# Performance work log

Measured on AMD Instinct MI355X. Metric: run time of the kernel, lower is better.

The kernel has to match this reference:

```python
import jax, jax.numpy as jnp
import numpy as np

D_MODEL = 512
NUM_HEADS = 8


def setup_inputs() -> dict:
    key = jax.random.key(0)
    ks = jax.random.split(key, 12)
    B, S, D = 2, 4096, D_MODEL
    scale = 1.0 / np.sqrt(D)
    inp = {
        "q": jax.random.normal(ks[0], (B, S, D), jnp.float32),
        "k": jax.random.normal(ks[1], (B, S, D), jnp.float32),
        "v": jax.random.normal(ks[2], (B, S, D), jnp.float32),
        "w_q": jax.random.normal(ks[3], (D, D), jnp.float32) * scale,
        "b_q": jax.random.normal(ks[4], (D,), jnp.float32) * scale,
        "w_k": jax.random.normal(ks[5], (D, D), jnp.float32) * scale,
        "b_k": jax.random.normal(ks[6], (D,), jnp.float32) * scale,
        "w_v": jax.random.normal(ks[7], (D, D), jnp.float32) * scale,
        "b_v": jax.random.normal(ks[8], (D,), jnp.float32) * scale,
        "w_o": jax.random.normal(ks[9], (D, D), jnp.float32) * scale,
        "b_o": jax.random.normal(ks[10], (D,), jnp.float32) * scale,
    }
    return inp


def _split_heads(x, h):
    b, s, d = x.shape
    return x.reshape(b, s, h, d // h).transpose(0, 2, 1, 3)  # [B,H,S,dk]


def reference(q, k, v, w_q, b_q, w_k, b_k, w_v, b_v, w_o, b_o):
    h = NUM_HEADS
    # Linear projections (torch Linear: x @ W.T + b)
    qh = _split_heads(q @ w_q.T + b_q, h)
    kh = _split_heads(k @ w_k.T + b_k, h)
    vh = _split_heads(v @ w_v.T + b_v, h)
    d_k = kh.shape[-1]
    scores = jnp.einsum("bhsd,bhtd->bhst", qh, kh) / jnp.sqrt(jnp.float32(d_k))
    attn = jax.nn.softmax(scores, axis=-1)  # [B,H,S,S] - materialized, as in source
    out = jnp.einsum("bhst,bhtd->bhsd", attn, vh)
    b, _, s, dk = out.shape
    out = out.transpose(0, 2, 1, 3).reshape(b, s, h * dk)
    return out @ w_o.T + b_o
```

## Files before the change

kernel.cpp:

```cpp
#include <hip/hip_runtime.h>
#include <hip/hip_bf16.h>

#define D_MODEL 512
#define NHEAD   8
#define DK      64
#define SEQ     4096
#define BATCH   2
#define NTOK    (BATCH * SEQ)

typedef __bf16 bf16;
typedef __bf16 bf16x2 __attribute__((ext_vector_type(2)));
typedef __bf16 bf16x4 __attribute__((ext_vector_type(4)));
typedef __bf16 bf16x8 __attribute__((ext_vector_type(8)));
typedef float  f32x4  __attribute__((ext_vector_type(4)));
typedef float  f32x16 __attribute__((ext_vector_type(16)));
typedef unsigned u32x4 __attribute__((ext_vector_type(4)));

#define MFMA16(a, b, c) __builtin_amdgcn_mfma_f32_16x16x32_bf16((a), (b), (c), 0, 0, 0)
#define MFMA32(a, b, c) __builtin_amdgcn_mfma_f32_32x32x16_bf16((a), (b), (c), 0, 0, 0)

#define QSCALE 0.18033688f

__device__ __forceinline__ unsigned pkbf16(float a, float b) {
    bf16x2 t = {(bf16)a, (bf16)b};
    return __builtin_bit_cast(unsigned, t);
}

__global__ __launch_bounds__(256) void cvt_w(
    const float* __restrict__ wq, const float* __restrict__ wk,
    const float* __restrict__ wv, const float* __restrict__ wo,
    bf16* __restrict__ Wb)
{
    int i = blockIdx.x * 256 + threadIdx.x;
    int m = i >> 16;
    int g = i & 65535;
    const float* src = (m == 0) ? wq : (m == 1) ? wk : (m == 2) ? wv : wo;
    float4 x = *(const float4*)(src + (size_t)g * 4);
    bf16x4 y = {(bf16)x.x, (bf16)x.y, (bf16)x.z, (bf16)x.w};
    *(bf16x4*)(Wb + (size_t)m * D_MODEL * D_MODEL + (size_t)g * 4) = y;
}

__global__ __launch_bounds__(256, 3) void proj_qkv(
    const float* __restrict__ q, const float* __restrict__ k, const float* __restrict__ v,
    const bf16* __restrict__ Wb,
    const float* __restrict__ bq, const float* __restrict__ bk, const float* __restrict__ bv,
    bf16* __restrict__ Qh, bf16* __restrict__ Kh, bf16* __restrict__ Vt)
{
    const int p = blockIdx.z;
    const float* X    = (p == 0) ? q  : (p == 1) ? k  : v;
    const bf16*  W    = Wb + (size_t)p * D_MODEL * D_MODEL;
    const float* bias = (p == 0) ? bq : (p == 1) ? bk : bv;

    __shared__ union __align__(16) {
        struct { bf16 As[128][72]; bf16 Bs[128][72]; } g;
        bf16 T[128][136];
    } sm;

    const int m0   = blockIdx.x * 128;
    const int n0   = blockIdx.y * 128;
    const int tid  = threadIdx.x;
    const int lane = tid & 63;
    const int wave = tid >> 6;
    const int low4 = lane & 15;
    const int quad = lane >> 4;
    const int wm   = wave >> 1;
    const int wn   = wave & 1;

    int srow[8], sc4[8];
    for (int it = 0; it < 8; ++it) {
        int idx = tid + it * 256;
        srow[it] = idx >> 4;
        sc4[it]  = (idx & 15) * 4;
    }
    int br[4], bc[4];
    for (int it = 0; it < 4; ++it) {
        int idx = tid + it * 256;
        br[it] = idx >> 3;
        bc[it] = (idx & 7) * 8;
    }

    float4 gA[8];
    bf16x8 gB[4];
    for (int it = 0; it < 8; ++it)
        gA[it] = *(const float4*)(X + (size_t)(m0 + srow[it]) * D_MODEL + sc4[it]);
    for (int it = 0; it < 4; ++it)
        gB[it] = *(const bf16x8*)(W + (size_t)(n0 + br[it]) * D_MODEL + bc[it]);

    f32x4 acc[4][4];
    for (int i = 0; i < 4; ++i)
        for (int j = 0; j < 4; ++j)
            acc[i][j] = f32x4{0.f, 0.f, 0.f, 0.f};

    for (int k0 = 0; k0 < D_MODEL; k0 += 64) {
        __syncthreads();
        for (int it = 0; it < 8; ++it) {
            bf16x4 wa = {(bf16)gA[it].x, (bf16)gA[it].y, (bf16)gA[it].z, (bf16)gA[it].w};
            *(bf16x4*)&sm.g.As[srow[it]][sc4[it]] = wa;
        }
        for (int it = 0; it < 4; ++it)
            *(bf16x8*)&sm.g.Bs[br[it]][bc[it]] = gB[it];
        __syncthreads();

        if (k0 + 64 < D_MODEL) {
            for (int it = 0; it < 8; ++it)
                gA[it] = *(const float4*)(X + (size_t)(m0 + srow[it]) * D_MODEL + k0 + 64 + sc4[it]);
            for (int it = 0; it < 4; ++it)
                gB[it] = *(const bf16x8*)(W + (size_t)(n0 + br[it]) * D_MODEL + k0 + 64 + bc[it]);
        }

        for (int ks = 0; ks < 2; ++ks) {
            bf16x8 a[4], b[4];
            for (int i = 0; i < 4; ++i)
                a[i] = *(const bf16x8*)&sm.g.As[wm * 64 + i * 16 + low4][ks * 32 + quad * 8];
            for (int j = 0; j < 4; ++j)
                b[j] = *(const bf16x8*)&sm.g.Bs[wn * 64 + j * 16 + low4][ks * 32 + quad * 8];
            for (int i = 0; i < 4; ++i)
                for (int j = 0; j < 4; ++j)
                    acc[i][j] = MFMA16(a[i], b[j], acc[i][j]);
        }
    }

    if (p < 2) {
        bf16* Out = (p == 0) ? Qh : Kh;
        const float sc = (p == 0) ? QSCALE : 1.0f;
        for (int j = 0; j < 4; ++j) {
            int col = n0 + wn * 64 + j * 16 + low4;
            float bcol = bias[col];
            for (int i = 0; i < 4; ++i)
                for (int r = 0; r < 4; ++r) {
                    int row = m0 + wm * 64 + i * 16 + quad * 4 + r;
                    Out[(size_t)row * D_MODEL + col] = (bf16)((acc[i][j][r] + bcol) * sc);
                }
        }
    } else {
        __syncthreads();
        for (int j = 0; j < 4; ++j) {
            int col = n0 + wn * 64 + j * 16 + low4;
            float bcol = bias[col];
            for (int i = 0; i < 4; ++i)
                for (int r = 0; r < 4; ++r)
                    sm.T[wn * 64 + j * 16 + low4][wm * 64 + i * 16 + quad * 4 + r] =
                        (bf16)(acc[i][j][r] + bcol);
        }
        __syncthreads();
        const int bb = m0 >> 12;
        const int s0 = (m0 & 4095);
        for (int it = 0; it < 8; ++it) {
            int cc = it * 16 + (tid >> 4);
            int ml = (tid & 15) * 8;
            int col = n0 + cc;
            int hh = col >> 6, dd = col & 63;
            *(bf16x8*)&Vt[(((size_t)(bb * NHEAD + hh) * DK + dd) << 12) + s0 + ml] =
                *(const bf16x8*)&sm.T[cc][ml];
        }
    }
}

__global__ __launch_bounds__(512, 2) void attn(
    const bf16* __restrict__ Qh, const bf16* __restrict__ Kh,
    const bf16* __restrict__ Vt, bf16* __restrict__ O)
{
    __shared__ union __align__(16) {
        struct { bf16 Ks[128][72]; bf16 Vs[64][136]; } s;
        float Obuf[4][32][68];
    } sm;
    __shared__ float Lbuf[4][32];

    const int q0   = blockIdx.x * 128;
    const int bh   = blockIdx.y;
    const int b    = bh >> 3, h = bh & 7;
    const int tid  = threadIdx.x;
    const int lane = tid & 63;
    const int wave = tid >> 6;
    const int qg   = wave >> 1;
    const int kg   = wave & 1;
    const int m32  = lane & 31;
    const int hl   = lane >> 5;

    const bf16* Kbase = Kh + (size_t)b * SEQ * D_MODEL + h * DK;
    const bf16* Vbase = Vt + (size_t)bh * DK * SEQ;

    const bf16* Qrow = Qh + (size_t)(b * SEQ + q0 + qg * 32 + m32) * D_MODEL + h * DK;
    bf16x8 qf[4];
    for (int ks = 0; ks < 4; ++ks)
        qf[ks] = *(const bf16x8*)(Qrow + ks * 16 + hl * 8);

    float l = 0.f;
    f32x16 acc[2];
    for (int i = 0; i < 16; ++i) { acc[0][i] = 0.f; acc[1][i] = 0.f; }

    int kr[2], kc[2], vr[2], vc[2];
    for (int it = 0; it < 2; ++it) {
        int c = tid + it * 512;
        kr[it] = c >> 3;  kc[it] = (c & 7) * 8;
        vr[it] = c >> 4;  vc[it] = (c & 15) * 8;
    }
    bf16x8 gk[2], gv[2];
    for (int it = 0; it < 2; ++it) {
        gk[it] = *(const bf16x8*)(Kbase + (size_t)kr[it] * D_MODEL + kc[it]);
        gv[it] = *(const bf16x8*)(Vbase + (size_t)vr[it] * SEQ + vc[it]);
    }

    for (int t0 = 0; t0 < SEQ; t0 += 128) {
        __syncthreads();
        for (int it = 0; it < 2; ++it) {
            *(bf16x8*)&sm.s.Ks[kr[it]][kc[it]] = gk[it];
            *(bf16x8*)&sm.s.Vs[vr[it]][vc[it]] = gv[it];
        }
        __syncthreads();

        if (t0 + 128 < SEQ) {
            for (int it = 0; it < 2; ++it) {
                gk[it] = *(const bf16x8*)(Kbase + (size_t)(t0 + 128 + kr[it]) * D_MODEL + kc[it]);
                gv[it] = *(const bf16x8*)(Vbase + (size_t)vr[it] * SEQ + t0 + 128 + vc[it]);
            }
        }

        for (int mt = 0; mt < 2; ++mt) {
            f32x16 sc;
            for (int i = 0; i < 16; ++i) sc[i] = 0.f;
            for (int ks = 0; ks < 4; ++ks) {
                bf16x8 kf = *(const bf16x8*)&sm.s.Ks[kg * 64 + mt * 32 + m32][ks * 16 + hl * 8];
                sc = MFMA32(kf, qf[ks], sc);
            }

            u32x4 pa, pb;
            {
                float p0 = __builtin_amdgcn_exp2f(sc[0]);
                float p1 = __builtin_amdgcn_exp2f(sc[1]);
                float p2 = __builtin_amdgcn_exp2f(sc[2]);
                float p3 = __builtin_amdgcn_exp2f(sc[3]);
                l += (p0 + p1) + (p2 + p3);
                unsigned y0 = pkbf16(p0, p1), y1 = pkbf16(p2, p3);
                p0 = __builtin_amdgcn_exp2f(sc[4]);
                p1 = __builtin_amdgcn_exp2f(sc[5]);
                p2 = __builtin_amdgcn_exp2f(sc[6]);
                p3 = __builtin_amdgcn_exp2f(sc[7]);
                l += (p0 + p1) + (p2 + p3);
                unsigned y2 = pkbf16(p0, p1), y3 = pkbf16(p2, p3);
                auto s0 = __builtin_amdgcn_permlane32_swap(y0, y2, false, false);
                auto s1 = __builtin_amdgcn_permlane32_swap(y1, y3, false, false);
                pa[0] = s0[0]; pa[2] = s0[1]; pa[1] = s1[0]; pa[3] = s1[1];

                p0 = __builtin_amdgcn_exp2f(sc[8]);
                p1 = __builtin_amdgcn_exp2f(sc[9]);
                p2 = __builtin_amdgcn_exp2f(sc[10]);
                p3 = __builtin_amdgcn_exp2f(sc[11]);
                l += (p0 + p1) + (p2 + p3);
                y0 = pkbf16(p0, p1); y1 = pkbf16(p2, p3);
                p0 = __builtin_amdgcn_exp2f(sc[12]);
                p1 = __builtin_amdgcn_exp2f(sc[13]);
                p2 = __builtin_amdgcn_exp2f(sc[14]);
                p3 = __builtin_amdgcn_exp2f(sc[15]);
                l += (p0 + p1) + (p2 + p3);
                y2 = pkbf16(p0, p1); y3 = pkbf16(p2, p3);
                auto s2 = __builtin_amdgcn_permlane32_swap(y0, y2, false, false);
                auto s3 = __builtin_amdgcn_permlane32_swap(y1, y3, false, false);
                pb[0] = s2[0]; pb[2] = s2[1]; pb[1] = s3[0]; pb[3] = s3[1];
            }
            bf16x8 pfa = __builtin_bit_cast(bf16x8, pa);
            bf16x8 pfb = __builtin_bit_cast(bf16x8, pb);

            for (int nt = 0; nt < 2; ++nt) {
                bf16x8 va = *(const bf16x8*)&sm.s.Vs[nt * 32 + m32][kg * 64 + (2 * mt) * 16 + hl * 8];
                acc[nt] = MFMA32(pfa, va, acc[nt]);
                bf16x8 vb = *(const bf16x8*)&sm.s.Vs[nt * 32 + m32][kg * 64 + (2 * mt + 1) * 16 + hl * 8];
                acc[nt] = MFMA32(pfb, vb, acc[nt]);
            }
        }
    }

    l += __shfl_xor(l, 32);
    __syncthreads();
    if (kg == 1) {
        for (int nt = 0; nt < 2; ++nt)
            for (int r = 0; r < 16; ++r) {
                int qq = (r & 3) + 8 * (r >> 2) + 4 * hl;
                sm.Obuf[qg][qq][nt * 32 + m32] = acc[nt][r];
            }
        if (hl == 0) Lbuf[qg][m32] = l;
    }
    __syncthreads();
    if (kg == 0) {
        float lt  = l + Lbuf[qg][m32];
        float inv = 1.0f / lt;
        for (int nt = 0; nt < 2; ++nt)
            for (int r = 0; r < 16; ++r) {
                int qq = (r & 3) + 8 * (r >> 2) + 4 * hl;
                float val = acc[nt][r] + sm.Obuf[qg][qq][nt * 32 + m32];
                float iv  = __shfl(inv, qq);
                O[(size_t)(b * SEQ + q0 + qg * 32 + qq) * D_MODEL + h * DK + nt * 32 + m32] =
                    (bf16)(val * iv);
            }
    }
}

__global__ __launch_bounds__(256, 4) void proj_out(
    const bf16* __restrict__ Oin, const bf16* __restrict__ Wo,
    const float* __restrict__ bo, float* __restrict__ out)
{
    __shared__ bf16 As[64][72];
    __shared__ bf16 Bs[64][72];

    const int m0   = blockIdx.x * 64;
    const int n0   = blockIdx.y * 64;
    const int tid  = threadIdx.x;
    const int lane = tid & 63;
    const int wave = tid >> 6;
    const int low4 = lane & 15;
    const int quad = lane >> 4;
    const int wm   = wave >> 1;
    const int wn   = wave & 1;

    int arow[2], ag[2];
    for (int it = 0; it < 2; ++it) {
        int idx = tid + it * 256;
        arow[it] = idx >> 3;
        ag[it]   = (idx & 7) * 8;
    }

    bf16x8 gA[2], gB[2];
    for (int it = 0; it < 2; ++it) {
        gA[it] = *(const bf16x8*)(Oin + (size_t)(m0 + arow[it]) * D_MODEL + ag[it]);
        gB[it] = *(const bf16x8*)(Wo + (size_t)(n0 + arow[it]) * D_MODEL + ag[it]);
    }

    f32x4 acc[2][2];
    for (int i = 0; i < 2; ++i)
        for (int j = 0; j < 2; ++j)
            acc[i][j] = f32x4{0.f, 0.f, 0.f, 0.f};

    for (int k0 = 0; k0 < D_MODEL; k0 += 64) {
        __syncthreads();
        for (int it = 0; it < 2; ++it) {
            *(bf16x8*)&As[arow[it]][ag[it]] = gA[it];
            *(bf16x8*)&Bs[arow[it]][ag[it]] = gB[it];
        }
        __syncthreads();

        if (k0 + 64 < D_MODEL) {
            for (int it = 0; it < 2; ++it) {
                gA[it] = *(const bf16x8*)(Oin + (size_t)(m0 + arow[it]) * D_MODEL + k0 + 64 + ag[it]);
                gB[it] = *(const bf16x8*)(Wo + (size_t)(n0 + arow[it]) * D_MODEL + k0 + 64 + ag[it]);
            }
        }

        for (int ks = 0; ks < 2; ++ks) {
            bf16x8 a[2], b[2];
            for (int i = 0; i < 2; ++i)
                a[i] = *(const bf16x8*)&As[wm * 32 + i * 16 + low4][ks * 32 + quad * 8];
            for (int j = 0; j < 2; ++j)
                b[j] = *(const bf16x8*)&Bs[wn * 32 + j * 16 + low4][ks * 32 + quad * 8];
            for (int i = 0; i < 2; ++i)
                for (int j = 0; j < 2; ++j)
                    acc[i][j] = MFMA16(a[i], b[j], acc[i][j]);
        }
    }

    for (int j = 0; j < 2; ++j) {
        int col = n0 + wn * 32 + j * 16 + low4;
        float bcol = bo[col];
        for (int i = 0; i < 2; ++i)
            for (int r = 0; r < 4; ++r) {
                int row = m0 + wm * 32 + i * 16 + quad * 4 + r;
                out[(size_t)row * D_MODEL + col] = acc[i][j][r] + bcol;
            }
    }
}

extern "C" void kernel_launch(void* const* d_in, const int* in_sizes, int n_in,
                              void* d_out, int out_size, void* d_ws, size_t ws_size,
                              hipStream_t stream)
{
    const float* q  = (const float*)d_in[0];
    const float* k  = (const float*)d_in[1];
    const float* v  = (const float*)d_in[2];
    const float* wq = (const float*)d_in[3];
    const float* bq = (const float*)d_in[4];
    const float* wk = (const float*)d_in[5];
    const float* bk = (const float*)d_in[6];
    const float* wv = (const float*)d_in[7];
    const float* bv = (const float*)d_in[8];
    const float* wo = (const float*)d_in[9];
    const float* bo = (const float*)d_in[10];

    const size_t NT = (size_t)NTOK * D_MODEL;
    bf16* Qh = (bf16*)d_ws;
    bf16* Kh = Qh + NT;
    bf16* Vt = Kh + NT;
    bf16* O  = Vt + NT;
    bf16* Wb = O + NT;

    cvt_w<<<1024, 256, 0, stream>>>(wq, wk, wv, wo, Wb);

    dim3 g1(NTOK / 128, D_MODEL / 128, 3);
    proj_qkv<<<g1, 256, 0, stream>>>(q, k, v, Wb, bq, bk, bv, Qh, Kh, Vt);

    dim3 g2(SEQ / 128, BATCH * NHEAD);
    attn<<<g2, 512, 0, stream>>>(Qh, Kh, Vt, O);

    dim3 g3(NTOK / 64, D_MODEL / 64);
    proj_out<<<g3, 256, 0, stream>>>(O, Wb + (size_t)3 * D_MODEL * D_MODEL, bo, (float*)d_out);
}
```

Baseline: 238.2 us.

## Fuse weight bf16 conversion into projection GEMMs and batch P·V MFMAs

Removes the separate weight-conversion kernel launch, so the projection kernels load fp32 weights directly and convert them to bf16 while staging into shared memory. In the attention inner loop, the softmax probabilities for both score subtiles are computed first, and all P·V MFMAs are then issued together, grouped by key chunk. The first change saves a launch and a weight round trip, but doubles the bytes read for weights in each GEMM tile. The second change raises live register pressure and aims to give better MFMA and LDS scheduling.

```diff
diff --git a/kernel.cpp b/kernel.cpp
--- a/kernel.cpp
+++ b/kernel.cpp
@@ -26,29 +26,15 @@
     return __builtin_bit_cast(unsigned, t);
 }
 
-__global__ __launch_bounds__(256) void cvt_w(
-    const float* __restrict__ wq, const float* __restrict__ wk,
-    const float* __restrict__ wv, const float* __restrict__ wo,
-    bf16* __restrict__ Wb)
-{
-    int i = blockIdx.x * 256 + threadIdx.x;
-    int m = i >> 16;
-    int g = i & 65535;
-    const float* src = (m == 0) ? wq : (m == 1) ? wk : (m == 2) ? wv : wo;
-    float4 x = *(const float4*)(src + (size_t)g * 4);
-    bf16x4 y = {(bf16)x.x, (bf16)x.y, (bf16)x.z, (bf16)x.w};
-    *(bf16x4*)(Wb + (size_t)m * D_MODEL * D_MODEL + (size_t)g * 4) = y;
-}
-
 __global__ __launch_bounds__(256, 3) void proj_qkv(
     const float* __restrict__ q, const float* __restrict__ k, const float* __restrict__ v,
-    const bf16* __restrict__ Wb,
+    const float* __restrict__ wq, const float* __restrict__ wk, const float* __restrict__ wv,
     const float* __restrict__ bq, const float* __restrict__ bk, const float* __restrict__ bv,
     bf16* __restrict__ Qh, bf16* __restrict__ Kh, bf16* __restrict__ Vt)
 {
     const int p = blockIdx.z;
     const float* X    = (p == 0) ? q  : (p == 1) ? k  : v;
-    const bf16*  W    = Wb + (size_t)p * D_MODEL * D_MODEL;
+    const float* W    = (p == 0) ? wq : (p == 1) ? wk : wv;
     const float* bias = (p == 0) ? bq : (p == 1) ? bk : bv;
 
     __shared__ union __align__(16) {
@@ -80,11 +66,14 @@
     }
 
     float4 gA[8];
-    bf16x8 gB[4];
+    float4 gB0[4], gB1[4];
     for (int it = 0; it < 8; ++it)
         gA[it] = *(const float4*)(X + (size_t)(m0 + srow[it]) * D_MODEL + sc4[it]);
-    for (int it = 0; it < 4; ++it)
-        gB[it] = *(const bf16x8*)(W + (size_t)(n0 + br[it]) * D_MODEL + bc[it]);
+    for (int it = 0; it < 4; ++it) {
+        const float* src = W + (size_t)(n0 + br[it]) * D_MODEL + bc[it];
+        gB0[it] = *(const float4*)src;
+        gB1[it] = *(const float4*)(src + 4);
+    }
 
     f32x4 acc[4][4];
     for (int i = 0; i < 4; ++i)
@@ -97,15 +86,21 @@
             bf16x4 wa = {(bf16)gA[it].x, (bf16)gA[it].y, (bf16)gA[it].z, (bf16)gA[it].w};
             *(bf16x4*)&sm.g.As[srow[it]][sc4[it]] = wa;
         }
-        for (int it = 0; it < 4; ++it)
-            *(bf16x8*)&sm.g.Bs[br[it]][bc[it]] = gB[it];
+        for (int it = 0; it < 4; ++it) {
+            bf16x8 wb = {(bf16)gB0[it].x, (bf16)gB0[it].y, (bf16)gB0[it].z, (bf16)gB0[it].w,
+                         (bf16)gB1[it].x, (bf16)gB1[it].y, (bf16)gB1[it].z, (bf16)gB1[it].w};
+            *(bf16x8*)&sm.g.Bs[br[it]][bc[it]] = wb;
+        }
         __syncthreads();
 
         if (k0 + 64 < D_MODEL) {
             for (int it = 0; it < 8; ++it)
                 gA[it] = *(const float4*)(X + (size_t)(m0 + srow[it]) * D_MODEL + k0 + 64 + sc4[it]);
-            for (int it = 0; it < 4; ++it)
-                gB[it] = *(const bf16x8*)(W + (size_t)(n0 + br[it]) * D_MODEL + k0 + 64 + bc[it]);
+            for (int it = 0; it < 4; ++it) {
+                const float* src = W + (size_t)(n0 + br[it]) * D_MODEL + k0 + 64 + bc[it];
+                gB0[it] = *(const float4*)src;
+                gB1[it] = *(const float4*)(src + 4);
+            }
         }
 
         for (int ks = 0; ks < 2; ++ks) {
@@ -216,6 +211,7 @@
             }
         }
 
+        u32x4 pf00, pf01, pf10, pf11;
         for (int mt = 0; mt < 2; ++mt) {
             f32x16 sc;
             for (int i = 0; i < 16; ++i) sc[i] = 0.f;
@@ -258,14 +254,30 @@
                 auto s3 = __builtin_amdgcn_permlane32_swap(y1, y3, false, false);
                 pb[0] = s2[0]; pb[2] = s2[1]; pb[1] = s3[0]; pb[3] = s3[1];
             }
-            bf16x8 pfa = __builtin_bit_cast(bf16x8, pa);
-            bf16x8 pfb = __builtin_bit_cast(bf16x8, pb);
-
+            if (mt == 0) { pf00 = pa; pf01 = pb; }
+            else         { pf10 = pa; pf11 = pb; }
+        }
+
+        {
+            bf16x8 p0 = __builtin_bit_cast(bf16x8, pf00);
+            bf16x8 p1 = __builtin_bit_cast(bf16x8, pf01);
+            bf16x8 p2 = __builtin_bit_cast(bf16x8, pf10);
+            bf16x8 p3 = __builtin_bit_cast(bf16x8, pf11);
             for (int nt = 0; nt < 2; ++nt) {
-                bf16x8 va = *(const bf16x8*)&sm.s.Vs[nt * 32 + m32][kg * 64 + (2 * mt) * 16 + hl * 8];
-                acc[nt] = MFMA32(pfa, va, acc[nt]);
-                bf16x8 vb = *(const bf16x8*)&sm.s.Vs[nt * 32 + m32][kg * 64 + (2 * mt + 1) * 16 + hl * 8];
-                acc[nt] = MFMA32(pfb, vb, acc[nt]);
+                bf16x8 v0 = *(const bf16x8*)&sm.s.Vs[nt * 32 + m32][kg * 64 + 0 * 16 + hl * 8];
+                acc[nt] = MFMA32(p0, v0, acc[nt]);
+            }
+            for (int nt = 0; nt < 2; ++nt) {
+                bf16x8 v1 = *(const bf16x8*)&sm.s.Vs[nt * 32 + m32][kg * 64 + 1 * 16 + hl * 8];
+                acc[nt] = MFMA32(p1, v1, acc[nt]);
+            }
+            for (int nt = 0; nt < 2; ++nt) {
+                bf16x8 v2 = *(const bf16x8*)&sm.s.Vs[nt * 32 + m32][kg * 64 + 2 * 16 + hl * 8];
+                acc[nt] = MFMA32(p2, v2, acc[nt]);
+            }
+            for (int nt = 0; nt < 2; ++nt) {
+                bf16x8 v3 = *(const bf16x8*)&sm.s.Vs[nt * 32 + m32][kg * 64 + 3 * 16 + hl * 8];
+                acc[nt] = MFMA32(p3, v3, acc[nt]);
             }
         }
     }
@@ -296,7 +308,7 @@
 }
 
 __global__ __launch_bounds__(256, 4) void proj_out(
-    const bf16* __restrict__ Oin, const bf16* __restrict__ Wo,
+    const bf16* __restrict__ Oin, const float* __restrict__ Wo,
     const float* __restrict__ bo, float* __restrict__ out)
 {
     __shared__ bf16 As[64][72];
@@ -319,10 +331,13 @@
         ag[it]   = (idx & 7) * 8;
     }
 
-    bf16x8 gA[2], gB[2];
+    bf16x8 gA[2];
+    float4 gB0[2], gB1[2];
     for (int it = 0; it < 2; ++it) {
         gA[it] = *(const bf16x8*)(Oin + (size_t)(m0 + arow[it]) * D_MODEL + ag[it]);
-        gB[it] = *(const bf16x8*)(Wo + (size_t)(n0 + arow[it]) * D_MODEL + ag[it]);
+        const float* src = Wo + (size_t)(n0 + arow[it]) * D_MODEL + ag[it];
+        gB0[it] = *(const float4*)src;
+        gB1[it] = *(const float4*)(src + 4);
     }
 
     f32x4 acc[2][2];
@@ -334,14 +349,18 @@
         __syncthreads();
         for (int it = 0; it < 2; ++it) {
             *(bf16x8*)&As[arow[it]][ag[it]] = gA[it];
-            *(bf16x8*)&Bs[arow[it]][ag[it]] = gB[it];
+            bf16x8 wb = {(bf16)gB0[it].x, (bf16)gB0[it].y, (bf16)gB0[it].z, (bf16)gB0[it].w,
+                         (bf16)gB1[it].x, (bf16)gB1[it].y, (bf16)gB1[it].z, (bf16)gB1[it].w};
+            *(bf16x8*)&Bs[arow[it]][ag[it]] = wb;
         }
         __syncthreads();
 
         if (k0 + 64 < D_MODEL) {
             for (int it = 0; it < 2; ++it) {
                 gA[it] = *(const bf16x8*)(Oin + (size_t)(m0 + arow[it]) * D_MODEL + k0 + 64 + ag[it]);
-                gB[it] = *(const bf16x8*)(Wo + (size_t)(n0 + arow[it]) * D_MODEL + k0 + 64 + ag[it]);
+                const float* src = Wo + (size_t)(n0 + arow[it]) * D_MODEL + k0 + 64 + ag[it];
+                gB0[it] = *(const float4*)src;
+                gB1[it] = *(const float4*)(src + 4);
             }
         }
 
@@ -389,16 +408,13 @@
     bf16* Kh = Qh + NT;
     bf16* Vt = Kh + NT;
     bf16* O  = Vt + NT;
-    bf16* Wb = O + NT;
-
-    cvt_w<<<1024, 256, 0, stream>>>(wq, wk, wv, wo, Wb);
 
     dim3 g1(NTOK / 128, D_MODEL / 128, 3);
-    proj_qkv<<<g1, 256, 0, stream>>>(q, k, v, Wb, bq, bk, bv, Qh, Kh, Vt);
+    proj_qkv<<<g1, 256, 0, stream>>>(q, k, v, wq, wk, wv, bq, bk, bv, Qh, Kh, Vt);
 
     dim3 g2(SEQ / 128, BATCH * NHEAD);
     attn<<<g2, 512, 0, stream>>>(Qh, Kh, Vt, O);
 
     dim3 g3(NTOK / 64, D_MODEL / 64);
-    proj_out<<<g3, 256, 0, stream>>>(O, Wb + (size_t)3 * D_MODEL * D_MODEL, bo, (float*)d_out);
+    proj_out<<<g3, 256, 0, stream>>>(O, wo, bo, (float*)d_out);
 }
```

New measurement: 244.7 us. +2.7%, slower.

## Process two query subtiles per wave in attention to reuse K/V tiles

Applied to the files above, without the earlier changes.

Doubles the query tile per attention block from 128 to 256 rows, with each wave computing scores and PV accumulation for two 32-row query subtiles sharing the same K and V fragments from LDS. This halves the K/V global and shared-memory traffic per query and the number of blocks launched. It increases register pressure (four accumulators, two score tiles) and reduces the grid to 256 blocks, which may lower occupancy and latency hiding.

```diff
diff --git a/kernel.cpp b/kernel.cpp
--- a/kernel.cpp
+++ b/kernel.cpp
@@ -24,6 +24,41 @@
 __device__ __forceinline__ unsigned pkbf16(float a, float b) {
     bf16x2 t = {(bf16)a, (bf16)b};
     return __builtin_bit_cast(unsigned, t);
+}
+
+__device__ __forceinline__ void softmax_pack(const f32x16& sc, float& l,
+                                             u32x4& pa, u32x4& pb) {
+    float p0 = __builtin_amdgcn_exp2f(sc[0]);
+    float p1 = __builtin_amdgcn_exp2f(sc[1]);
+    float p2 = __builtin_amdgcn_exp2f(sc[2]);
+    float p3 = __builtin_amdgcn_exp2f(sc[3]);
+    l += (p0 + p1) + (p2 + p3);
+    unsigned y0 = pkbf16(p0, p1), y1 = pkbf16(p2, p3);
+    p0 = __builtin_amdgcn_exp2f(sc[4]);
+    p1 = __builtin_amdgcn_exp2f(sc[5]);
+    p2 = __builtin_amdgcn_exp2f(sc[6]);
+    p3 = __builtin_amdgcn_exp2f(sc[7]);
+    l += (p0 + p1) + (p2 + p3);
+    unsigned y2 = pkbf16(p0, p1), y3 = pkbf16(p2, p3);
+    auto s0 = __builtin_amdgcn_permlane32_swap(y0, y2, false, false);
+    auto s1 = __builtin_amdgcn_permlane32_swap(y1, y3, false, false);
+    pa[0] = s0[0]; pa[2] = s0[1]; pa[1] = s1[0]; pa[3] = s1[1];
+
+    p0 = __builtin_amdgcn_exp2f(sc[8]);
+    p1 = __builtin_amdgcn_exp2f(sc[9]);
+    p2 = __builtin_amdgcn_exp2f(sc[10]);
+    p3 = __builtin_amdgcn_exp2f(sc[11]);
+    l += (p0 + p1) + (p2 + p3);
+    y0 = pkbf16(p0, p1); y1 = pkbf16(p2, p3);
+    p0 = __builtin_amdgcn_exp2f(sc[12]);
+    p1 = __builtin_amdgcn_exp2f(sc[13]);
+    p2 = __builtin_amdgcn_exp2f(sc[14]);
+    p3 = __builtin_amdgcn_exp2f(sc[15]);
+    l += (p0 + p1) + (p2 + p3);
+    y2 = pkbf16(p0, p1); y3 = pkbf16(p2, p3);
+    auto s2 = __builtin_amdgcn_permlane32_swap(y0, y2, false, false);
+    auto s3 = __builtin_amdgcn_permlane32_swap(y1, y3, false, false);
+    pb[0] = s2[0]; pb[2] = s2[1]; pb[1] = s3[0]; pb[3] = s3[1];
 }
 
 __global__ __launch_bounds__(256) void cvt_w(
@@ -166,7 +201,7 @@
     } sm;
     __shared__ float Lbuf[4][32];
 
-    const int q0   = blockIdx.x * 128;
+    const int q0   = blockIdx.x * 256;
     const int bh   = blockIdx.y;
     const int b    = bh >> 3, h = bh & 7;
     const int tid  = threadIdx.x;
@@ -180,22 +215,31 @@
     const bf16* Kbase = Kh + (size_t)b * SEQ * D_MODEL + h * DK;
     const bf16* Vbase = Vt + (size_t)bh * DK * SEQ;
 
-    const bf16* Qrow = Qh + (size_t)(b * SEQ + q0 + qg * 32 + m32) * D_MODEL + h * DK;
-    bf16x8 qf[4];
-    for (int ks = 0; ks < 4; ++ks)
-        qf[ks] = *(const bf16x8*)(Qrow + ks * 16 + hl * 8);
-
-    float l = 0.f;
-    f32x16 acc[2];
-    for (int i = 0; i < 16; ++i) { acc[0][i] = 0.f; acc[1][i] = 0.f; }
+    const bf16* Qrow0 = Qh + (size_t)(b * SEQ + q0 + qg * 64 + m32) * D_MODEL + h * DK;
+    const bf16* Qrow1 = Qrow0 + (size_t)32 * D_MODEL;
+    bf16x8 qf0[4], qf1[4];
+#pragma unroll
+    for (int ks = 0; ks < 4; ++ks) {
+        qf0[ks] = *(const bf16x8*)(Qrow0 + ks * 16 + hl * 8);
+        qf1[ks] = *(const bf16x8*)(Qrow1 + ks * 16 + hl * 8);
+    }
+
+    float l0 = 0.f, l1 = 0.f;
+    f32x16 acc00, acc01, acc10, acc11;
+#pragma unroll
+    for (int i = 0; i < 16; ++i) {
+        acc00[i] = 0.f; acc01[i] = 0.f; acc10[i] = 0.f; acc11[i] = 0.f;
+    }
 
     int kr[2], kc[2], vr[2], vc[2];
+#pragma unroll
     for (int it = 0; it < 2; ++it) {
         int c = tid + it * 512;
         kr[it] = c >> 3;  kc[it] = (c & 7) * 8;
         vr[it] = c >> 4;  vc[it] = (c & 15) * 8;
     }
     bf16x8 gk[2], gv[2];
+#pragma unroll
     for (int it = 0; it < 2; ++it) {
         gk[it] = *(const bf16x8*)(Kbase + (size_t)kr[it] * D_MODEL + kc[it]);
         gv[it] = *(const bf16x8*)(Vbase + (size_t)vr[it] * SEQ + vc[it]);
@@ -203,6 +247,7 @@
 
     for (int t0 = 0; t0 < SEQ; t0 += 128) {
         __syncthreads();
+#pragma unroll
         for (int it = 0; it < 2; ++it) {
             *(bf16x8*)&sm.s.Ks[kr[it]][kc[it]] = gk[it];
             *(bf16x8*)&sm.s.Vs[vr[it]][vc[it]] = gv[it];
@@ -210,88 +255,76 @@
         __syncthreads();
 
         if (t0 + 128 < SEQ) {
+#pragma unroll
             for (int it = 0; it < 2; ++it) {
                 gk[it] = *(const bf16x8*)(Kbase + (size_t)(t0 + 128 + kr[it]) * D_MODEL + kc[it]);
                 gv[it] = *(const bf16x8*)(Vbase + (size_t)vr[it] * SEQ + t0 + 128 + vc[it]);
             }
         }
 
+        u32x4 pq0[4], pq1[4];
+#pragma unroll
         for (int mt = 0; mt < 2; ++mt) {
-            f32x16 sc;
-            for (int i = 0; i < 16; ++i) sc[i] = 0.f;
+            f32x16 s0, s1;
+#pragma unroll
+            for (int i = 0; i < 16; ++i) { s0[i] = 0.f; s1[i] = 0.f; }
+#pragma unroll
             for (int ks = 0; ks < 4; ++ks) {
                 bf16x8 kf = *(const bf16x8*)&sm.s.Ks[kg * 64 + mt * 32 + m32][ks * 16 + hl * 8];
-                sc = MFMA32(kf, qf[ks], sc);
-            }
-
-            u32x4 pa, pb;
-            {
-                float p0 = __builtin_amdgcn_exp2f(sc[0]);
-                float p1 = __builtin_amdgcn_exp2f(sc[1]);
-                float p2 = __builtin_amdgcn_exp2f(sc[2]);
-                float p3 = __builtin_amdgcn_exp2f(sc[3]);
-                l += (p0 + p1) + (p2 + p3);
-                unsigned y0 = pkbf16(p0, p1), y1 = pkbf16(p2, p3);
-                p0 = __builtin_amdgcn_exp2f(sc[4]);
-                p1 = __builtin_amdgcn_exp2f(sc[5]);
-                p2 = __builtin_amdgcn_exp2f(sc[6]);
-                p3 = __builtin_amdgcn_exp2f(sc[7]);
-                l += (p0 + p1) + (p2 + p3);
-                unsigned y2 = pkbf16(p0, p1), y3 = pkbf16(p2, p3);
-                auto s0 = __builtin_amdgcn_permlane32_swap(y0, y2, false, false);
-                auto s1 = __builtin_amdgcn_permlane32_swap(y1, y3, false, false);
-                pa[0] = s0[0]; pa[2] = s0[1]; pa[1] = s1[0]; pa[3] = s1[1];
-
-                p0 = __builtin_amdgcn_exp2f(sc[8]);
-                p1 = __builtin_amdgcn_exp2f(sc[9]);
-                p2 = __builtin_amdgcn_exp2f(sc[10]);
-                p3 = __builtin_amdgcn_exp2f(sc[11]);
-                l += (p0 + p1) + (p2 + p3);
-                y0 = pkbf16(p0, p1); y1 = pkbf16(p2, p3);
-                p0 = __builtin_amdgcn_exp2f(sc[12]);
-                p1 = __builtin_amdgcn_exp2f(sc[13]);
-                p2 = __builtin_amdgcn_exp2f(sc[14]);
-                p3 = __builtin_amdgcn_exp2f(sc[15]);
-                l += (p0 + p1) + (p2 + p3);
-                y2 = pkbf16(p0, p1); y3 = pkbf16(p2, p3);
-                auto s2 = __builtin_amdgcn_permlane32_swap(y0, y2, false, false);
-                auto s3 = __builtin_amdgcn_permlane32_swap(y1, y3, false, false);
-                pb[0] = s2[0]; pb[2] = s2[1]; pb[1] = s3[0]; pb[3] = s3[1];
-            }
-            bf16x8 pfa = __builtin_bit_cast(bf16x8, pa);
-            bf16x8 pfb = __builtin_bit_cast(bf16x8, pb);
-
-            for (int nt = 0; nt < 2; ++nt) {
-                bf16x8 va = *(const bf16x8*)&sm.s.Vs[nt * 32 + m32][kg * 64 + (2 * mt) * 16 + hl * 8];
-                acc[nt] = MFMA32(pfa, va, acc[nt]);
-                bf16x8 vb = *(const bf16x8*)&sm.s.Vs[nt * 32 + m32][kg * 64 + (2 * mt + 1) * 16 + hl * 8];
-                acc[nt] = MFMA32(pfb, vb, acc[nt]);
-            }
-        }
-    }
-
-    l += __shfl_xor(l, 32);
-    __syncthreads();
-    if (kg == 1) {
-        for (int nt = 0; nt < 2; ++nt)
+                s0 = MFMA32(kf, qf0[ks], s0);
+                s1 = MFMA32(kf, qf1[ks], s1);
+            }
+            u32x4 a0, b0, a1, b1;
+            softmax_pack(s0, l0, a0, b0);
+            softmax_pack(s1, l1, a1, b1);
+            pq0[2 * mt] = a0; pq0[2 * mt + 1] = b0;
+            pq1[2 * mt] = a1; pq1[2 * mt + 1] = b1;
+        }
+
+#pragma unroll
+        for (int ksl = 0; ksl < 4; ++ksl) {
+            bf16x8 pA = __builtin_bit_cast(bf16x8, pq0[ksl]);
+            bf16x8 pB = __builtin_bit_cast(bf16x8, pq1[ksl]);
+            bf16x8 v0 = *(const bf16x8*)&sm.s.Vs[0 * 32 + m32][kg * 64 + ksl * 16 + hl * 8];
+            acc00 = MFMA32(pA, v0, acc00);
+            acc10 = MFMA32(pB, v0, acc10);
+            bf16x8 v1 = *(const bf16x8*)&sm.s.Vs[1 * 32 + m32][kg * 64 + ksl * 16 + hl * 8];
+            acc01 = MFMA32(pA, v1, acc01);
+            acc11 = MFMA32(pB, v1, acc11);
+        }
+    }
+
+    l0 += __shfl_xor(l0, 32);
+    l1 += __shfl_xor(l1, 32);
+
+#pragma unroll
+    for (int qs = 0; qs < 2; ++qs) {
+        float l = (qs == 0) ? l0 : l1;
+        __syncthreads();
+        if (kg == 1) {
+#pragma unroll
             for (int r = 0; r < 16; ++r) {
                 int qq = (r & 3) + 8 * (r >> 2) + 4 * hl;
-                sm.Obuf[qg][qq][nt * 32 + m32] = acc[nt][r];
-            }
-        if (hl == 0) Lbuf[qg][m32] = l;
-    }
-    __syncthreads();
-    if (kg == 0) {
-        float lt  = l + Lbuf[qg][m32];
-        float inv = 1.0f / lt;
-        for (int nt = 0; nt < 2; ++nt)
+                sm.Obuf[qg][qq][0 * 32 + m32] = (qs == 0) ? acc00[r] : acc10[r];
+                sm.Obuf[qg][qq][1 * 32 + m32] = (qs == 0) ? acc01[r] : acc11[r];
+            }
+            if (hl == 0) Lbuf[qg][m32] = l;
+        }
+        __syncthreads();
+        if (kg == 0) {
+            float lt  = l + Lbuf[qg][m32];
+            float inv = 1.0f / lt;
+#pragma unroll
             for (int r = 0; r < 16; ++r) {
                 int qq = (r & 3) + 8 * (r >> 2) + 4 * hl;
-                float val = acc[nt][r] + sm.Obuf[qg][qq][nt * 32 + m32];
-                float iv  = __shfl(inv, qq);
-                O[(size_t)(b * SEQ + q0 + qg * 32 + qq) * D_MODEL + h * DK + nt * 32 + m32] =
-                    (bf16)(val * iv);
-            }
+                float v0 = ((qs == 0) ? acc00[r] : acc10[r]) + sm.Obuf[qg][qq][0 * 32 + m32];
+                float v1 = ((qs == 0) ? acc01[r] : acc11[r]) + sm.Obuf[qg][qq][1 * 32 + m32];
+                float iv = __shfl(inv, qq);
+                size_t row = (size_t)(b * SEQ + q0 + qg * 64 + qs * 32 + qq);
+                O[row * D_MODEL + h * DK + 0 * 32 + m32] = (bf16)(v0 * iv);
+                O[row * D_MODEL + h * DK + 1 * 32 + m32] = (bf16)(v1 * iv);
+            }
+        }
     }
 }
 
@@ -396,7 +429,7 @@
     dim3 g1(NTOK / 128, D_MODEL / 128, 3);
     proj_qkv<<<g1, 256, 0, stream>>>(q, k, v, Wb, bq, bk, bv, Qh, Kh, Vt);
 
-    dim3 g2(SEQ / 128, BATCH * NHEAD);
+    dim3 g2(SEQ / 256, BATCH * NHEAD);
     attn<<<g2, 512, 0, stream>>>(Qh, Kh, Vt, O);
 
     dim3 g3(NTOK / 64, D_MODEL / 64);
```

Result: faster. 216.4 us (-9.1%).
